# Kernel optimization log

Hardware: AMD Instinct MI355X
Metric: run time of the kernel (lower is better)

Reference implementation:

```python
import jax, jax.numpy as jnp
import numpy as np

MARGIN = 1.0   # TripletLoss(margin) init arg
EPS = 1e-6     # torch F.pairwise_distance eps used by nn.TripletMarginLoss
INF = 1e9

N, D_EMB, N_CLASSES = 8192, 1024, 128


def setup_inputs() -> dict:
    key = jax.random.key(0)
    k1, k2 = jax.random.split(key)
    embeddings = jax.random.normal(k1, (N, D_EMB), dtype=jnp.float32)
    target = jax.random.randint(k2, (N,), 0, N_CLASSES, dtype=jnp.int64 if jax.config.jax_enable_x64 else jnp.int32)
    return {"embeddings": embeddings, "target": target}


def _mine_and_loss(embeddings, target):
    # Vectorized, deterministic equivalent of the per-anchor random mining loop:
    # full pairwise L2 distance matrix via a GEMM (compute-bound core).
    sq = jnp.sum(embeddings * embeddings, axis=1)                      # [N]
    d2 = sq[:, None] + sq[None, :] - 2.0 * (embeddings @ embeddings.T)  # [N, N]
    Dm = jnp.sqrt(jnp.maximum(d2, 0.0))                                 # [N, N]

    same = target[:, None] == target[None, :]
    eye = jnp.eye(target.shape[0], dtype=bool)
    pos_mask = same & ~eye          # valid positives (same class, not self)
    neg_mask = ~same                # valid negatives (different class)

    # Positive: hardest (farthest) same-class sample (deterministic stand-in
    # for the original's random positive draw).
    pos_scores = jnp.where(pos_mask, Dm, -INF)
    pos_idx = jnp.argmax(pos_scores, axis=1)                           # [N]
    d_p = jnp.max(pos_scores, axis=1)                                  # [N]

    # Negative: semi-hard (d_p < d_n < d_p + margin), pick the closest such
    # negative; if none exists, fall back to the overall hardest (min-dist)
    # negative -- mirrors the loop's early-break vs. min_dist fallback.
    semi = neg_mask & (Dm > d_p[:, None]) & (Dm < (d_p + MARGIN)[:, None])
    has_semi = jnp.any(semi, axis=1)
    neg_semi = jnp.argmin(jnp.where(semi, Dm, INF), axis=1)
    neg_hard = jnp.argmin(jnp.where(neg_mask, Dm, INF), axis=1)
    neg_idx = jnp.where(has_semi, neg_semi, neg_hard)                  # [N]

    # nn.TripletMarginLoss(margin, p=2): mean(relu(d(a,p) - d(a,n) + margin))
    # with torch's pairwise_distance eps added to the difference.
    a = embeddings
    p = embeddings[pos_idx]
    n = embeddings[neg_idx]
    dp = jnp.sqrt(jnp.sum((a - p + EPS) ** 2, axis=1))
    dn = jnp.sqrt(jnp.sum((a - n + EPS) ** 2, axis=1))
    return jnp.mean(jax.nn.relu(dp - dn + MARGIN))


def reference(embeddings, target):
    return _mine_and_loss(embeddings, target)
```

## Files before the change

kernel.cpp:

```cpp
#include <hip/hip_runtime.h>
#include <hip/hip_bf16.h>

#define N 8192
#define D 1024
#define MARGIN 1.0f
#define EPS 1e-6f

typedef __attribute__((ext_vector_type(8))) short bf16x8;
typedef __attribute__((ext_vector_type(4))) float f32x4;
typedef __attribute__((ext_vector_type(8))) _Float16 f16x8;
typedef __attribute__((ext_vector_type(4))) _Float16 f16x4;
typedef __attribute__((ext_vector_type(8))) unsigned short u16x8;

__device__ inline unsigned short f2bf(float x) {
    unsigned u = __float_as_uint(x);
    unsigned r = (u + 0x7FFFu + ((u >> 16) & 1u)) >> 16;
    return (unsigned short)r;
}

__device__ inline float h2f(unsigned hb) {
    return (float)__builtin_bit_cast(_Float16, (unsigned short)hb);
}

__global__ __launch_bounds__(256) void prep_kernel(const float* __restrict__ E,
                                                   unsigned short* __restrict__ Ebf,
                                                   float* __restrict__ sq) {
    const int r = blockIdx.x;
    const int tid = threadIdx.x;
    const float4 v = ((const float4*)(E + (size_t)r * D))[tid];
    ushort4 o;
    o.x = f2bf(v.x); o.y = f2bf(v.y); o.z = f2bf(v.z); o.w = f2bf(v.w);
    ((ushort4*)(Ebf + (size_t)r * D))[tid] = o;
    float s = v.x * v.x + v.y * v.y + v.z * v.z + v.w * v.w;
    for (int off = 32; off > 0; off >>= 1) s += __shfl_down(s, off);
    __shared__ float red[4];
    const int lane = tid & 63, wave = tid >> 6;
    if (lane == 0) red[wave] = s;
    __syncthreads();
    if (tid == 0) sq[r] = red[0] + red[1] + red[2] + red[3];
}

__global__ __launch_bounds__(256) void cls_kernel(const int* __restrict__ target,
                                                  unsigned char* __restrict__ cls) {
    const int t = blockIdx.x * 256 + threadIdx.x;
    cls[t] = (unsigned char)target[t];
}


#define SLOT_0A0 0
#define SLOT_0A1 16384
#define SLOT_0B0 32768
#define SLOT_0B1 49152
#define SLOT_1A0 65536
#define SLOT_1A1 81920
#define SLOT_1B0 98304
#define SLOT_1B1 114688

#define STAGE(slotOff, baseRow, kcol) do {                                              \
    const unsigned short* _s0 = E + (size_t)((baseRow) + (tid >> 2)) * D + (kcol) + stc * 8; \
    __builtin_amdgcn_global_load_lds(                                                    \
        (const __attribute__((address_space(1))) unsigned int*)_s0,                      \
        (__attribute__((address_space(3))) unsigned int*)(smem + (slotOff) + wave * 1024), 16, 0, 0); \
    const unsigned short* _s1 = _s0 + (size_t)128 * D;                                   \
    __builtin_amdgcn_global_load_lds(                                                    \
        (const __attribute__((address_space(1))) unsigned int*)_s1,                      \
        (__attribute__((address_space(3))) unsigned int*)(smem + (slotOff) + 8192 + wave * 1024), 16, 0, 0); \
} while (0)

#define PHASE(b, ks, mq, LOADB, SLOT_ST, TILE_ST, BASE_ST, KH_ST, DO_VM) do {            \
    const char* _As = smem + (b) * 65536 + (ks) * 16384;                                 \
    const char* _Bs = smem + (b) * 65536 + 32768 + (ks) * 16384;                         \
    if (LOADB) {                                                                         \
        _Pragma("unroll") for (int nj = 0; nj < 4; ++nj)                                 \
            bfr[nj] = *(const bf16x8*)(_Bs + (wn * 64 + nj * 16 + mr) * 64 + swz);       \
    }                                                                                    \
    bf16x8 af[4];                                                                        \
    _Pragma("unroll") for (int mi = 0; mi < 4; ++mi)                                     \
        af[mi] = *(const bf16x8*)(_As + (wm * 128 + (mq) * 64 + mi * 16 + mr) * 64 + swz); \
    STAGE(SLOT_ST, BASE_ST, (TILE_ST) * 64 + (KH_ST));                                   \
    __builtin_amdgcn_s_setprio(1);                                                       \
    _Pragma("unroll") for (int mi = 0; mi < 4; ++mi)                                     \
        _Pragma("unroll") for (int nj = 0; nj < 4; ++nj)                                 \
            acc[(mq) * 4 + mi][nj] = __builtin_amdgcn_mfma_f32_16x16x32_bf16(            \
                af[mi], bfr[nj], acc[(mq) * 4 + mi][nj], 0, 0, 0);                       \
    __builtin_amdgcn_s_setprio(0);                                                       \
    if (DO_VM) __asm__ __volatile__("s_waitcnt vmcnt(6)" ::: "memory");                  \
    __asm__ __volatile__("s_barrier" ::: "memory");                                      \
} while (0)

__global__ __launch_bounds__(512, 2) void gemm_kernel(const unsigned short* __restrict__ E,
                                                      const float* __restrict__ sq,
                                                      _Float16* __restrict__ D2h) {
    extern __shared__ char smem[];

    const int tid = threadIdx.x;
    const int lane = tid & 63;
    const int wave = tid >> 6;
    const int wm = wave >> 2;
    const int wn = wave & 3;
    const int mr = lane & 15;
    const int q = lane >> 4;
    const int swz = ((q ^ ((mr >> 1) & 3)) << 4);
    const int stc = (tid & 3) ^ ((tid >> 3) & 3);

    const int h = blockIdx.x;
    const int l = (h & 7) * 62 + (h >> 3);

    int by = (int)((1.0f + sqrtf(8.0f * (float)l + 1.0f)) * 0.5f);
    while (by * (by - 1) / 2 > l) --by;
    while ((by + 1) * by / 2 <= l) ++by;
    const int bx = l - by * (by - 1) / 2;
    const int rm = by * 256;
    const int cn = bx * 256;

    f32x4 acc[8][4] = {};
    bf16x8 bfr[4];

    STAGE(SLOT_0A0, rm, 0);
    STAGE(SLOT_0B0, cn, 0);
    STAGE(SLOT_0A1, rm, 32);
    STAGE(SLOT_0B1, cn, 32);
    STAGE(SLOT_1A0, rm, 64);
    __asm__ __volatile__("s_waitcnt vmcnt(6)" ::: "memory");
    __asm__ __volatile__("s_barrier" ::: "memory");

    for (int i = 0; i < 8; ++i) {
        const int kt = 2 * i;
        const int t2 = (kt + 2 < 16) ? kt + 2 : 15;
        const int t3 = (kt + 3 < 16) ? kt + 3 : 15;
        PHASE(0, 0, 0, 1, SLOT_1B0, kt + 1, cn, 0, 0);
        PHASE(0, 0, 1, 0, SLOT_1A1, kt + 1, rm, 32, 1);
        PHASE(0, 1, 0, 1, SLOT_1B1, kt + 1, cn, 32, 0);
        PHASE(0, 1, 1, 0, SLOT_0A0, t2, rm, 0, 1);
        PHASE(1, 0, 0, 1, SLOT_0B0, t2, cn, 0, 0);
        PHASE(1, 0, 1, 0, SLOT_0A1, t2, rm, 32, 1);
        PHASE(1, 1, 0, 1, SLOT_0B1, t2, cn, 32, 0);
        PHASE(1, 1, 1, 0, SLOT_1A0, t3, rm, 0, 1);
    }

    const int crow = q * 4;
    float sqj[4];
#pragma unroll
    for (int nj = 0; nj < 4; ++nj) sqj[nj] = sq[cn + wn * 64 + nj * 16 + mr];
#pragma unroll
    for (int mg = 0; mg < 8; ++mg) {
        const int i0 = rm + wm * 128 + mg * 16 + crow;
        const f32x4 sqi = *(const f32x4*)(sq + i0);
#pragma unroll
        for (int nj = 0; nj < 4; ++nj) {
            const int j = cn + wn * 64 + nj * 16 + mr;
            f16x4 tv;
#pragma unroll
            for (int r = 0; r < 4; ++r) {
                const float d2 = fmaxf(sqi[r] + sqj[nj] - 2.0f * acc[mg][nj][r], 0.0f);
                const _Float16 h16 = (_Float16)d2;
                tv[r] = h16;
                D2h[(size_t)(i0 + r) * N + j] = h16;
            }
            *(f16x4*)(D2h + (size_t)j * N + i0) = tv;
        }
    }
}

__global__ __launch_bounds__(256) void gemm_diag_kernel(const unsigned short* __restrict__ E,
                                                        const float* __restrict__ sq,
                                                        _Float16* __restrict__ D2h) {
    __shared__ char smem[128 * 136 * 2];
    unsigned short* As = (unsigned short*)smem;
    unsigned short* Bs = (unsigned short*)(smem + 8192);
    _Float16* Ts = (_Float16*)smem;

    const int tid = threadIdx.x;
    const int lane = tid & 63;
    const int wave = tid >> 6;
    const int wm = wave & 1, wn = wave >> 1;

    const int c = blockIdx.x;
    const int t = c / 3, s = c - 3 * t;
    const int sm = (s + 1) >> 1;
    const int sn = s >> 1;
    const int rm = t * 256 + sm * 128;
    const int cn = t * 256 + sn * 128;
    const bool offdiag = (s == 1);

    const int srow = tid >> 2;
    const int scol = (tid & 3) * 8;

    const unsigned short* gA = E + (size_t)(rm + srow) * D + scol;
    const unsigned short* gB = E + (size_t)(cn + srow) * D + scol;

    f32x4 acc[4][4] = {};

    const int kq = (lane >> 4) * 8;
    const int mr = lane & 15;

    for (int k0 = 0; k0 < D; k0 += 32) {
        __builtin_amdgcn_global_load_lds(
            (const __attribute__((address_space(1))) unsigned int*)(gA + k0),
            (__attribute__((address_space(3))) unsigned int*)((char*)As + wave * 1024), 16, 0, 0);
        __builtin_amdgcn_global_load_lds(
            (const __attribute__((address_space(1))) unsigned int*)(gA + (size_t)64 * D + k0),
            (__attribute__((address_space(3))) unsigned int*)((char*)As + 4096 + wave * 1024), 16, 0, 0);
        __builtin_amdgcn_global_load_lds(
            (const __attribute__((address_space(1))) unsigned int*)(gB + k0),
            (__attribute__((address_space(3))) unsigned int*)((char*)Bs + wave * 1024), 16, 0, 0);
        __builtin_amdgcn_global_load_lds(
            (const __attribute__((address_space(1))) unsigned int*)(gB + (size_t)64 * D + k0),
            (__attribute__((address_space(3))) unsigned int*)((char*)Bs + 4096 + wave * 1024), 16, 0, 0);
        __syncthreads();

        bf16x8 af[4], bfr[4];
#pragma unroll
        for (int mi = 0; mi < 4; ++mi)
            af[mi] = *(const bf16x8*)(As + (wm * 64 + mi * 16 + mr) * 32 + kq);
#pragma unroll
        for (int ni = 0; ni < 4; ++ni)
            bfr[ni] = *(const bf16x8*)(Bs + (wn * 64 + ni * 16 + mr) * 32 + kq);
#pragma unroll
        for (int mi = 0; mi < 4; ++mi)
#pragma unroll
            for (int ni = 0; ni < 4; ++ni)
                acc[mi][ni] = __builtin_amdgcn_mfma_f32_16x16x32_bf16(af[mi], bfr[ni], acc[mi][ni], 0, 0, 0);
        __syncthreads();
    }

    const int crow = (lane >> 4) * 4;
    const int ccol = lane & 15;
    float sqj[4];
#pragma unroll
    for (int ni = 0; ni < 4; ++ni)
        sqj[ni] = sq[cn + wn * 64 + ni * 16 + ccol];
#pragma unroll
    for (int mi = 0; mi < 4; ++mi) {
        const int lrow = wm * 64 + mi * 16 + crow;
        const int i0 = rm + lrow;
        float sqi[4];
#pragma unroll
        for (int r = 0; r < 4; ++r) sqi[r] = sq[i0 + r];
#pragma unroll
        for (int ni = 0; ni < 4; ++ni) {
            const int lcol = wn * 64 + ni * 16 + ccol;
            const int j = cn + lcol;
            f16x4 tv;
#pragma unroll
            for (int r = 0; r < 4; ++r) {
                float d2 = fmaxf(sqi[r] + sqj[ni] - 2.0f * acc[mi][ni][r], 0.0f);
                _Float16 h = (_Float16)d2;
                D2h[(size_t)(i0 + r) * N + j] = h;
                tv[r] = h;
            }
            if (offdiag)
                *(f16x4*)(Ts + (size_t)lcol * 136 + lrow) = tv;
        }
    }
    if (offdiag) {
        __syncthreads();
#pragma unroll
        for (int it = 0; it < 8; ++it) {
            const int rt = it * 16 + (tid >> 4);
            const int seg = tid & 15;
            f16x8 v = *(const f16x8*)(Ts + (size_t)rt * 136 + seg * 8);
            *(f16x8*)(D2h + (size_t)(cn + rt) * N + rm + seg * 8) = v;
        }
    }
}

__global__ __launch_bounds__(256) void mine_kernel(const _Float16* __restrict__ D2h,
                                                   const unsigned char* __restrict__ cls,
                                                   float* __restrict__ loss_arr) {
    const int i = blockIdx.x;
    const int tid = threadIdx.x;
    const int lane = tid & 63, wave = tid >> 6;
    const unsigned tcb = cls[i];
    const unsigned short* row = (const unsigned short*)(D2h + (size_t)i * N);

    u16x8 v[4];
    unsigned long long c8[4];
#pragma unroll
    for (int it = 0; it < 4; ++it) {
        v[it] = *(const u16x8*)(row + it * 2048 + tid * 8);
        c8[it] = *(const unsigned long long*)(cls + it * 2048 + tid * 8);
    }

    unsigned pm = 0u, nm = 0xFFFFu;
#pragma unroll
    for (int it = 0; it < 4; ++it) {
#pragma unroll
        for (int e = 0; e < 8; ++e) {
            const unsigned hb = v[it][e];
            const bool s = ((unsigned)(c8[it] >> (8 * e)) & 0xFFu) == tcb;
            pm = max(pm, s ? hb : 0u);
            nm = min(nm, s ? 0xFFFFu : hb);
        }
    }
    for (int off = 1; off < 64; off <<= 1) {
        pm = max(pm, (unsigned)__shfl_xor((int)pm, off));
        nm = min(nm, (unsigned)__shfl_xor((int)nm, off));
    }
    __shared__ unsigned redp[4], redn[4], reds[4];
    if (lane == 0) { redp[wave] = pm; redn[wave] = nm; }
    __syncthreads();
    pm = max(max(redp[0], redp[1]), max(redp[2], redp[3]));
    nm = min(min(redn[0], redn[1]), min(redn[2], redn[3]));
    const unsigned lob = pm;

    unsigned sm = 0xFFFFu;
#pragma unroll
    for (int it = 0; it < 4; ++it) {
#pragma unroll
        for (int e = 0; e < 8; ++e) {
            const unsigned hb = v[it][e];
            sm = min(sm, hb > lob ? hb : 0xFFFFu);
        }
    }
    for (int off = 1; off < 64; off <<= 1)
        sm = min(sm, (unsigned)__shfl_xor((int)sm, off));
    if (lane == 0) reds[wave] = sm;
    __syncthreads();
    if (tid == 0) {
        sm = min(min(reds[0], reds[1]), min(reds[2], reds[3]));
        const float lo = h2f(lob);
        const float dp = sqrtf(lo);
        const float hw = dp + MARGIN;
        const float hi = hw * hw;
        const float smv = h2f(sm);
        const float dn2 = (smv < hi) ? smv : h2f(nm);
        loss_arr[i] = fmaxf(dp - sqrtf(dn2) + MARGIN, 0.0f);
    }
}

__global__ __launch_bounds__(256) void reduce_kernel(const float* __restrict__ loss_arr,
                                                     float* __restrict__ out) {
    const int tid = threadIdx.x;
    float s = 0.0f;
    for (int k = tid; k < N; k += 256) s += loss_arr[k];
    for (int off = 32; off > 0; off >>= 1) s += __shfl_down(s, off);
    __shared__ float red[4];
    const int lane = tid & 63, wave = tid >> 6;
    if (lane == 0) red[wave] = s;
    __syncthreads();
    if (tid == 0) out[0] = (red[0] + red[1] + red[2] + red[3]) * (1.0f / N);
}

extern "C" void kernel_launch(void* const* d_in, const int* in_sizes, int n_in,
                              void* d_out, int out_size, void* d_ws, size_t ws_size,
                              hipStream_t stream) {
    const float* E = (const float*)d_in[0];
    const int* target = (const int*)d_in[1];
    float* out = (float*)d_out;
    char* ws = (char*)d_ws;

    unsigned short* Ebf = (unsigned short*)ws;
    float* sq        = (float*)(ws + (size_t)16777216);
    float* loss_arr  = (float*)(ws + (size_t)16809984);
    unsigned char* cls = (unsigned char*)(ws + (size_t)16842752);
    _Float16* D2h    = (_Float16*)(ws + (size_t)16875520);

    static bool attr_set = false;
    if (!attr_set) {
        hipFuncSetAttribute((const void*)gemm_kernel,
                            hipFuncAttributeMaxDynamicSharedMemorySize, 131072);
        attr_set = true;
    }

    prep_kernel<<<N, 256, 0, stream>>>(E, Ebf, sq);
    cls_kernel<<<N / 256, 256, 0, stream>>>(target, cls);
    gemm_kernel<<<496, 512, 131072, stream>>>(Ebf, sq, D2h);
    gemm_diag_kernel<<<96, 256, 0, stream>>>(Ebf, sq, D2h);
    mine_kernel<<<N, 256, 0, stream>>>(D2h, cls, loss_arr);
    reduce_kernel<<<1, 256, 0, stream>>>(loss_arr, out);
}
```

Before: 216.3 us.

## Fold diagonal GEMM tiles into main kernel, stage transpose via LDS, merge cls prep

```diff
diff --git a/kernel.cpp b/kernel.cpp
--- a/kernel.cpp
+++ b/kernel.cpp
@@ -23,8 +23,10 @@
 }
 
 __global__ __launch_bounds__(256) void prep_kernel(const float* __restrict__ E,
+                                                   const int* __restrict__ target,
                                                    unsigned short* __restrict__ Ebf,
-                                                   float* __restrict__ sq) {
+                                                   float* __restrict__ sq,
+                                                   unsigned char* __restrict__ cls) {
     const int r = blockIdx.x;
     const int tid = threadIdx.x;
     const float4 v = ((const float4*)(E + (size_t)r * D))[tid];
@@ -37,13 +39,10 @@
     const int lane = tid & 63, wave = tid >> 6;
     if (lane == 0) red[wave] = s;
     __syncthreads();
-    if (tid == 0) sq[r] = red[0] + red[1] + red[2] + red[3];
-}
-
-__global__ __launch_bounds__(256) void cls_kernel(const int* __restrict__ target,
-                                                  unsigned char* __restrict__ cls) {
-    const int t = blockIdx.x * 256 + threadIdx.x;
-    cls[t] = (unsigned char)target[t];
+    if (tid == 0) {
+        sq[r] = red[0] + red[1] + red[2] + red[3];
+        cls[r] = (unsigned char)target[r];
+    }
 }
 
 
@@ -88,12 +87,111 @@
     __asm__ __volatile__("s_barrier" ::: "memory");                                      \
 } while (0)
 
+__device__ __forceinline__ void diag_path(char* smem,
+                                          const unsigned short* __restrict__ E,
+                                          const float* __restrict__ sq,
+                                          _Float16* __restrict__ D2h,
+                                          const int c, const int tid) {
+    const int lane = tid & 63;
+    const int wave = tid >> 6;
+    const int wmL = wave >> 2;
+    const int wnL = wave & 3;
+    const int mr = lane & 15;
+    const int q = lane >> 4;
+    const int kq = q * 8;
+
+    const int t = c / 3, s = c - 3 * t;
+    const int smi = (s + 1) >> 1;
+    const int sni = s >> 1;
+    const int rm = t * 256 + smi * 128;
+    const int cn = t * 256 + sni * 128;
+    const bool offdiag = (s == 1);
+
+    f32x4 acc[4][2] = {};
+
+#define DSTAGE(sl, kk) do {                                                              \
+    __builtin_amdgcn_global_load_lds(                                                    \
+        (const __attribute__((address_space(1))) unsigned int*)(E + (size_t)(rm + (tid >> 2)) * D + (kk) * 32 + (tid & 3) * 8), \
+        (__attribute__((address_space(3))) unsigned int*)(smem + (sl) * 32768 + wave * 1024), 16, 0, 0); \
+    __builtin_amdgcn_global_load_lds(                                                    \
+        (const __attribute__((address_space(1))) unsigned int*)(E + (size_t)(cn + (tid >> 2)) * D + (kk) * 32 + (tid & 3) * 8), \
+        (__attribute__((address_space(3))) unsigned int*)(smem + (sl) * 32768 + 16384 + wave * 1024), 16, 0, 0); \
+} while (0)
+
+    DSTAGE(0, 0);
+    DSTAGE(1, 1);
+    for (int k = 0; k < 32; ++k) {
+        const int kn = (k + 2 < 32) ? k + 2 : 31;
+        DSTAGE((k + 2) & 3, kn);
+        __asm__ __volatile__("s_waitcnt vmcnt(4)" ::: "memory");
+        __asm__ __volatile__("s_barrier" ::: "memory");
+        const unsigned short* As = (const unsigned short*)(smem + (size_t)(k & 3) * 32768);
+        const unsigned short* Bs = As + 8192;
+        bf16x8 af[4], bfv[2];
+#pragma unroll
+        for (int mi = 0; mi < 4; ++mi)
+            af[mi] = *(const bf16x8*)(As + (wmL * 64 + mi * 16 + mr) * 32 + kq);
+#pragma unroll
+        for (int ni = 0; ni < 2; ++ni)
+            bfv[ni] = *(const bf16x8*)(Bs + (wnL * 32 + ni * 16 + mr) * 32 + kq);
+#pragma unroll
+        for (int mi = 0; mi < 4; ++mi)
+#pragma unroll
+            for (int ni = 0; ni < 2; ++ni)
+                acc[mi][ni] = __builtin_amdgcn_mfma_f32_16x16x32_bf16(af[mi], bfv[ni], acc[mi][ni], 0, 0, 0);
+    }
+#undef DSTAGE
+    __syncthreads();
+
+    _Float16* Ts = (_Float16*)smem;
+    float sqjL[2];
+#pragma unroll
+    for (int ni = 0; ni < 2; ++ni) sqjL[ni] = sq[cn + wnL * 32 + ni * 16 + mr];
+#pragma unroll
+    for (int mi = 0; mi < 4; ++mi) {
+        const int lrow = wmL * 64 + mi * 16 + q * 4;
+        const int i0 = rm + lrow;
+        const f32x4 sqi = *(const f32x4*)(sq + i0);
+#pragma unroll
+        for (int ni = 0; ni < 2; ++ni) {
+            const int lcol = wnL * 32 + ni * 16 + mr;
+            const int j = cn + lcol;
+            f16x4 tv;
+#pragma unroll
+            for (int r = 0; r < 4; ++r) {
+                const float d2 = fmaxf(sqi[r] + sqjL[ni] - 2.0f * acc[mi][ni][r], 0.0f);
+                const _Float16 h = (_Float16)d2;
+                D2h[(size_t)(i0 + r) * N + j] = h;
+                tv[r] = h;
+            }
+            if (offdiag)
+                *(f16x4*)(Ts + (size_t)lcol * 136 + lrow) = tv;
+        }
+    }
+    if (offdiag) {
+        __syncthreads();
+#pragma unroll
+        for (int it = 0; it < 4; ++it) {
+            const int rt = it * 32 + (tid >> 4);
+            const int seg = tid & 15;
+            f16x8 v = *(const f16x8*)(Ts + (size_t)rt * 136 + seg * 8);
+            *(f16x8*)(D2h + (size_t)(cn + rt) * N + rm + seg * 8) = v;
+        }
+    }
+}
+
 __global__ __launch_bounds__(512, 2) void gemm_kernel(const unsigned short* __restrict__ E,
                                                       const float* __restrict__ sq,
                                                       _Float16* __restrict__ D2h) {
     extern __shared__ char smem[];
 
     const int tid = threadIdx.x;
+
+    if (blockIdx.x >= 496) {
+        diag_path(smem, E, sq, D2h, blockIdx.x - 496, tid);
+        return;
+    }
+
     const int lane = tid & 63;
     const int wave = tid >> 6;
     const int wm = wave >> 2;
@@ -138,17 +236,24 @@
         PHASE(1, 1, 1, 0, SLOT_1A0, t3, rm, 0, 1);
     }
 
+    __asm__ __volatile__("s_waitcnt vmcnt(0) lgkmcnt(0)" ::: "memory");
+    __asm__ __volatile__("s_barrier" ::: "memory");
+
     const int crow = q * 4;
     float sqj[4];
 #pragma unroll
     for (int nj = 0; nj < 4; ++nj) sqj[nj] = sq[cn + wn * 64 + nj * 16 + mr];
 #pragma unroll
     for (int mg = 0; mg < 8; ++mg) {
-        const int i0 = rm + wm * 128 + mg * 16 + crow;
+        const int iloc = wm * 128 + mg * 16 + crow;
+        const int i0 = rm + iloc;
         const f32x4 sqi = *(const f32x4*)(sq + i0);
+        const unsigned cch = (unsigned)iloc >> 3;
+        const unsigned cof = ((unsigned)iloc & 7) << 1;
 #pragma unroll
         for (int nj = 0; nj < 4; ++nj) {
-            const int j = cn + wn * 64 + nj * 16 + mr;
+            const int jloc = wn * 64 + nj * 16 + mr;
+            const int j = cn + jloc;
             f16x4 tv;
 #pragma unroll
             for (int r = 0; r < 4; ++r) {
@@ -157,110 +262,19 @@
                 tv[r] = h16;
                 D2h[(size_t)(i0 + r) * N + j] = h16;
             }
-            *(f16x4*)(D2h + (size_t)j * N + i0) = tv;
-        }
-    }
-}
-
-__global__ __launch_bounds__(256) void gemm_diag_kernel(const unsigned short* __restrict__ E,
-                                                        const float* __restrict__ sq,
-                                                        _Float16* __restrict__ D2h) {
-    __shared__ char smem[128 * 136 * 2];
-    unsigned short* As = (unsigned short*)smem;
-    unsigned short* Bs = (unsigned short*)(smem + 8192);
-    _Float16* Ts = (_Float16*)smem;
-
-    const int tid = threadIdx.x;
-    const int lane = tid & 63;
-    const int wave = tid >> 6;
-    const int wm = wave & 1, wn = wave >> 1;
-
-    const int c = blockIdx.x;
-    const int t = c / 3, s = c - 3 * t;
-    const int sm = (s + 1) >> 1;
-    const int sn = s >> 1;
-    const int rm = t * 256 + sm * 128;
-    const int cn = t * 256 + sn * 128;
-    const bool offdiag = (s == 1);
-
-    const int srow = tid >> 2;
-    const int scol = (tid & 3) * 8;
-
-    const unsigned short* gA = E + (size_t)(rm + srow) * D + scol;
-    const unsigned short* gB = E + (size_t)(cn + srow) * D + scol;
-
-    f32x4 acc[4][4] = {};
-
-    const int kq = (lane >> 4) * 8;
-    const int mr = lane & 15;
-
-    for (int k0 = 0; k0 < D; k0 += 32) {
-        __builtin_amdgcn_global_load_lds(
-            (const __attribute__((address_space(1))) unsigned int*)(gA + k0),
-            (__attribute__((address_space(3))) unsigned int*)((char*)As + wave * 1024), 16, 0, 0);
-        __builtin_amdgcn_global_load_lds(
-            (const __attribute__((address_space(1))) unsigned int*)(gA + (size_t)64 * D + k0),
-            (__attribute__((address_space(3))) unsigned int*)((char*)As + 4096 + wave * 1024), 16, 0, 0);
-        __builtin_amdgcn_global_load_lds(
-            (const __attribute__((address_space(1))) unsigned int*)(gB + k0),
-            (__attribute__((address_space(3))) unsigned int*)((char*)Bs + wave * 1024), 16, 0, 0);
-        __builtin_amdgcn_global_load_lds(
-            (const __attribute__((address_space(1))) unsigned int*)(gB + (size_t)64 * D + k0),
-            (__attribute__((address_space(3))) unsigned int*)((char*)Bs + 4096 + wave * 1024), 16, 0, 0);
-        __syncthreads();
-
-        bf16x8 af[4], bfr[4];
-#pragma unroll
-        for (int mi = 0; mi < 4; ++mi)
-            af[mi] = *(const bf16x8*)(As + (wm * 64 + mi * 16 + mr) * 32 + kq);
-#pragma unroll
-        for (int ni = 0; ni < 4; ++ni)
-            bfr[ni] = *(const bf16x8*)(Bs + (wn * 64 + ni * 16 + mr) * 32 + kq);
-#pragma unroll
-        for (int mi = 0; mi < 4; ++mi)
-#pragma unroll
-            for (int ni = 0; ni < 4; ++ni)
-                acc[mi][ni] = __builtin_amdgcn_mfma_f32_16x16x32_bf16(af[mi], bfr[ni], acc[mi][ni], 0, 0, 0);
-        __syncthreads();
-    }
-
-    const int crow = (lane >> 4) * 4;
-    const int ccol = lane & 15;
-    float sqj[4];
-#pragma unroll
-    for (int ni = 0; ni < 4; ++ni)
-        sqj[ni] = sq[cn + wn * 64 + ni * 16 + ccol];
-#pragma unroll
-    for (int mi = 0; mi < 4; ++mi) {
-        const int lrow = wm * 64 + mi * 16 + crow;
-        const int i0 = rm + lrow;
-        float sqi[4];
-#pragma unroll
-        for (int r = 0; r < 4; ++r) sqi[r] = sq[i0 + r];
-#pragma unroll
-        for (int ni = 0; ni < 4; ++ni) {
-            const int lcol = wn * 64 + ni * 16 + ccol;
-            const int j = cn + lcol;
-            f16x4 tv;
-#pragma unroll
-            for (int r = 0; r < 4; ++r) {
-                float d2 = fmaxf(sqi[r] + sqj[ni] - 2.0f * acc[mi][ni][r], 0.0f);
-                _Float16 h = (_Float16)d2;
-                D2h[(size_t)(i0 + r) * N + j] = h;
-                tv[r] = h;
-            }
-            if (offdiag)
-                *(f16x4*)(Ts + (size_t)lcol * 136 + lrow) = tv;
-        }
-    }
-    if (offdiag) {
-        __syncthreads();
-#pragma unroll
-        for (int it = 0; it < 8; ++it) {
-            const int rt = it * 16 + (tid >> 4);
-            const int seg = tid & 15;
-            f16x8 v = *(const f16x8*)(Ts + (size_t)rt * 136 + seg * 8);
-            *(f16x8*)(D2h + (size_t)(cn + rt) * N + rm + seg * 8) = v;
+            *(f16x4*)(smem + (size_t)jloc * 512 + ((cch ^ (jloc & 31)) << 4) + cof) = tv;
+        }
+    }
+    __syncthreads();
+    {
+        const int jr = tid >> 1;
+        const int hf = tid & 1;
+        _Float16* dst = D2h + (size_t)(cn + jr) * N + rm + hf * 128;
+#pragma unroll
+        for (int st = 0; st < 16; ++st) {
+            const unsigned cc = (unsigned)(hf * 16 + st);
+            f16x8 v = *(const f16x8*)(smem + (size_t)jr * 512 + ((cc ^ (jr & 31)) << 4));
+            *(f16x8*)(dst + st * 8) = v;
         }
     }
 }
@@ -363,10 +377,8 @@
         attr_set = true;
     }
 
-    prep_kernel<<<N, 256, 0, stream>>>(E, Ebf, sq);
-    cls_kernel<<<N / 256, 256, 0, stream>>>(target, cls);
-    gemm_kernel<<<496, 512, 131072, stream>>>(Ebf, sq, D2h);
-    gemm_diag_kernel<<<96, 256, 0, stream>>>(Ebf, sq, D2h);
+    prep_kernel<<<N, 256, 0, stream>>>(E, target, Ebf, sq, cls);
+    gemm_kernel<<<592, 512, 131072, stream>>>(Ebf, sq, D2h);
     mine_kernel<<<N, 256, 0, stream>>>(D2h, cls, loss_arr);
     reduce_kernel<<<1, 256, 0, stream>>>(loss_arr, out);
 }
```

New measurement: 232.9 us. 1.08x slower.
